# Performance work log

Hardware: AMD Instinct MI355X
Metric: run time of the kernel (lower is better)

## Reference

```python
import jax, jax.numpy as jnp
import numpy as np

D_X, D_K, D_V = 1024, 128, 128
B, N = 8, 2048


def setup_inputs() -> dict:
    key = jax.random.key(0)
    ks = jax.random.split(key, 7)
    s = lambda fan_in: 1.0 / np.sqrt(fan_in)
    return {
        "x": jax.random.normal(ks[0], (B, N, D_X), dtype=jnp.float32),
        "w_q": jax.random.uniform(ks[1], (D_K, D_X), jnp.float32, -s(D_X), s(D_X)),
        "b_q": jax.random.uniform(ks[2], (D_K,), jnp.float32, -s(D_X), s(D_X)),
        "w_k": jax.random.uniform(ks[3], (D_K, D_X), jnp.float32, -s(D_X), s(D_X)),
        "b_k": jax.random.uniform(ks[4], (D_K,), jnp.float32, -s(D_X), s(D_X)),
        "w_v": jax.random.uniform(ks[5], (D_V, D_X), jnp.float32, -s(D_X), s(D_X)),
        "b_v": jax.random.uniform(ks[6], (D_V,), jnp.float32, -s(D_X), s(D_X)),
    }


def reference(x, w_q, b_q, w_k, b_k, w_v, b_v):
    # Q is computed in the original module but unused; omit (no effect on output).
    K = jnp.einsum('bnx,kx->bnk', x, w_k) + b_k  # [B,N,d_k]
    V = jnp.einsum('bnx,vx->bnv', x, w_v) + b_v  # [B,N,d_v]
    # logits = K @ V^T / sqrt(d_k)  -> [B,N,N]  (note: K vs V, not Q vs K)
    scale = 1.0 / np.sqrt(D_K).astype(np.float32)
    logits = jnp.einsum('bnk,bmk->bnm', K, V) * scale
    attn = jax.nn.softmax(logits, axis=-1)
    return jnp.einsum('bnm,bmv->bnv', attn, V)
```

## Files before the change

### kernel.cpp

```cpp
#include <hip/hip_runtime.h>
#include <hip/hip_bf16.h>


typedef short s16x8 __attribute__((ext_vector_type(8)));
typedef float f32x4 __attribute__((ext_vector_type(4)));
typedef unsigned short u16;

#define AS1 __attribute__((address_space(1)))
#define AS3 __attribute__((address_space(3)))

__device__ __forceinline__ void gld_lds16(const void* g, void* l) {
  __builtin_amdgcn_global_load_lds((const AS1 unsigned int*)g, (AS3 unsigned int*)l, 16, 0, 0);
}

__device__ __forceinline__ float bf2f(u16 u) {
  unsigned int v = ((unsigned int)u) << 16;
  return __builtin_bit_cast(float, v);
}
__device__ __forceinline__ u16 f2bf(float f) {
  unsigned int u = __builtin_bit_cast(unsigned int, f);
  u += 0x7fffu + ((u >> 16) & 1u);
  return (u16)(u >> 16);
}
__device__ __forceinline__ unsigned pack_bf2(float a, float b) {
  unsigned ua = __builtin_bit_cast(unsigned, a) + 0x8000u;
  unsigned ub = __builtin_bit_cast(unsigned, b) + 0x8000u;
  return __builtin_amdgcn_perm(ub, ua, 0x07060302u);
}

__global__ __launch_bounds__(256, 4) void wconv_kernel(
    const float* __restrict__ wk, const float* __restrict__ wv,
    u16* __restrict__ wbf)
{
  const int e = (blockIdx.x * 256 + threadIdx.x) * 8;
  const float* src = (e < 131072) ? (wk + e) : (wv + (e - 131072));
  float4 a = *(const float4*)src;
  float4 b = *(const float4*)(src + 4);
  union { unsigned u[4]; s16x8 v; } pk;
  pk.u[0] = pack_bf2(a.x, a.y); pk.u[1] = pack_bf2(a.z, a.w);
  pk.u[2] = pack_bf2(b.x, b.y); pk.u[3] = pack_bf2(b.z, b.w);
  *(s16x8*)(wbf + e) = pk.v;
}

__global__ __launch_bounds__(512, 2) void kv_gemm_kernel(
    const float* __restrict__ x, const u16* __restrict__ wbf,
    const float* __restrict__ bk, const float* __restrict__ bv,
    u16* __restrict__ Kout, u16* __restrict__ Vout, u16* __restrict__ VTout)
{
  __shared__ u16 sA[2][8 * 512];
  __shared__ u16 sB[4][32 * 512];

  const int tid  = threadIdx.x;
  const int wave = tid >> 6;
  const int lane = tid & 63;
  const int l16  = lane & 15;
  const int lq   = lane >> 4;
  const int row0 = blockIdx.x * 64;
  const int wr   = wave >> 2;
  const int wc   = wave & 3;

  f32x4 acc[2][4];
  for (int i = 0; i < 2; ++i)
    for (int j = 0; j < 4; ++j) acc[i][j] = (f32x4){0.f, 0.f, 0.f, 0.f};

  const int kc = tid & 7, arow = tid >> 3;
  const float* aSrc = x + (size_t)(row0 + arow) * 1024 + kc * 8;
  const int aSlot = (((arow >> 4) * 2 + (kc >> 2)) * 512) + ((kc & 3) * 16 + (arow & 15)) * 8;

  const u16* bSrc[4];
  for (int i = 0; i < 4; ++i) {
    const int sl = wave + i * 8;
    bSrc[i] = wbf + (size_t)((sl >> 1) * 16 + l16) * 1024 + (sl & 1) * 32 + lq * 8;
  }

  for (int i = 0; i < 4; ++i)
    gld_lds16(bSrc[i], &sB[0][(wave + i * 8) * 512]);
  float4 p0a = *(const float4*)(aSrc);
  float4 p0b = *(const float4*)(aSrc + 4);
  for (int i = 0; i < 4; ++i)
    gld_lds16(bSrc[i] + 64, &sB[1][(wave + i * 8) * 512]);
  float4 p1a = *(const float4*)(aSrc + 64);
  float4 p1b = *(const float4*)(aSrc + 68);

#pragma unroll
  for (int s = 0; s < 16; ++s) {
    const int buf2 = s & 1, buf4 = s & 3;
    {
      union { unsigned u[4]; s16x8 v; } pk;
      pk.u[0] = pack_bf2(p0a.x, p0a.y); pk.u[1] = pack_bf2(p0a.z, p0a.w);
      pk.u[2] = pack_bf2(p0b.x, p0b.y); pk.u[3] = pack_bf2(p0b.z, p0b.w);
      *(s16x8*)(&sA[buf2][aSlot]) = pk.v;
    }
    asm volatile("s_waitcnt lgkmcnt(0)" ::: "memory");
    __builtin_amdgcn_s_barrier();
    if (s == 15) asm volatile("s_waitcnt vmcnt(0)" ::: "memory");
    else         asm volatile("s_waitcnt vmcnt(6)" ::: "memory");
    __builtin_amdgcn_sched_barrier(0);

    if (s + 2 < 16) {
      for (int i = 0; i < 4; ++i)
        gld_lds16(bSrc[i] + (s + 2) * 64, &sB[(s + 2) & 3][(wave + i * 8) * 512]);
    }
    p0a = p1a; p0b = p1b;
    if (s + 2 < 16) {
      p1a = *(const float4*)(aSrc + (s + 2) * 64);
      p1b = *(const float4*)(aSrc + (s + 2) * 64 + 4);
    }

    s16x8 af[2][2], bfr[4][2];
    for (int rb = 0; rb < 2; ++rb)
      for (int ks = 0; ks < 2; ++ks)
        af[rb][ks] = *(const s16x8*)(&sA[buf2][(((wr * 2 + rb) * 2 + ks) * 64 + lane) * 8]);
    for (int cb = 0; cb < 4; ++cb)
      for (int ks = 0; ks < 2; ++ks)
        bfr[cb][ks] = *(const s16x8*)(&sB[buf4][(((wc * 4 + cb) * 2 + ks) * 64 + lane) * 8]);
    for (int rb = 0; rb < 2; ++rb)
      for (int cb = 0; cb < 4; ++cb)
        for (int ks = 0; ks < 2; ++ks)
          acc[rb][cb] = __builtin_amdgcn_mfma_f32_16x16x32_bf16(af[rb][ks], bfr[cb][ks], acc[rb][cb], 0, 0, 0);
  }

  const int  colBase = wc * 64;
  const bool isV = (wc >= 2);
  const float vscale = isV ? 1.0f : 0.08838834764831845f;
  u16* outN = isV ? Vout : Kout;
  float fbias[4];
  for (int cb = 0; cb < 4; ++cb) {
    const int col = colBase + cb * 16 + l16;
    fbias[cb] = isV ? bv[col - 128] : bk[col];
  }
  for (int rb = 0; rb < 2; ++rb) {
    const int grow0 = row0 + wr * 32 + rb * 16 + lq * 4;
    for (int cb = 0; cb < 4; ++cb) {
      const int gcol = colBase + cb * 16 + l16;
      const int ocol = isV ? (gcol - 128) : gcol;
      union { u16 u[4]; unsigned long long ull; } pk;
      for (int r = 0; r < 4; ++r) {
        u16 h = f2bf((acc[rb][cb][r] + fbias[cb]) * vscale);
        outN[(size_t)(grow0 + r) * 128 + ocol] = h;
        pk.u[r] = h;
      }
      if (isV) {
        const int bidx = grow0 >> 11;
        const int n    = grow0 & 2047;
        *(unsigned long long*)(VTout + (size_t)bidx * 128 * 2048 + (size_t)ocol * 2048 + n) = pk.ull;
      }
    }
  }
}

__global__ __launch_bounds__(256, 2) void flash_kernel(
    const u16* __restrict__ Kmat, const u16* __restrict__ Vmat,
    const u16* __restrict__ VT, float* __restrict__ out,
    float* __restrict__ Opart, float* __restrict__ lbuf)
{
  __shared__ u16 sV[2][16 * 512];
  __shared__ u16 sVT[2][16 * 512];

  const int tid  = threadIdx.x;
  const int wave = tid >> 6;
  const int lane = tid & 63;
  const int l16  = lane & 15;
  const int lq   = lane >> 4;
  const int b    = blockIdx.y;
  const int q0   = blockIdx.x * 64;
  const int z    = blockIdx.z;
  const int ntiles = (2048 / gridDim.z) / 64;
  const int mstart = z * (2048 / gridDim.z);

  const int bq   = lq & 1;
  const bool ahi = (lq & 2) != 0;
  const int src0 = l16 + (2 * bq + 0) * 16;
  const int src1 = l16 + (2 * bq + 1) * 16;

  s16x8 kf[4];
  {
    const u16* Kb = Kmat + ((size_t)b * 2048 + q0 + wave * 16 + l16) * 128 + lq * 8;
    for (int ks = 0; ks < 4; ++ks) kf[ks] = *(const s16x8*)(Kb + ks * 32);
  }

  const u16* vSrc[4];  const u16* vtSrc[4];
  {
    const u16* Vb  = Vmat + (size_t)b * 2048 * 128;
    const u16* VTb = VT   + (size_t)b * 128 * 2048;
    for (int i = 0; i < 4; ++i) {
      const int sl = wave + i * 4;
      vSrc[i]  = Vb  + (size_t)((sl >> 2) * 16 + l16) * 128 + (sl & 3) * 32 + lq * 8;
      vtSrc[i] = VTb + (size_t)((sl >> 1) * 16 + l16) * 2048 + (sl & 1) * 32 + lq * 8;
    }
  }

  f32x4 oacc[8];
  for (int v = 0; v < 8; ++v) oacc[v] = (f32x4){0.f, 0.f, 0.f, 0.f};
  float lrow = 0.f;

  for (int i = 0; i < 4; ++i) {
    gld_lds16(vSrc[i] + (size_t)mstart * 128, &sV[0][(wave + i * 4) * 512]);
    gld_lds16(vtSrc[i] + mstart,              &sVT[0][(wave + i * 4) * 512]);
  }

  for (int mt = 0; mt < ntiles; ++mt) {
    const int buf = mt & 1;
    asm volatile("s_barrier" ::: "memory");
    if (mt + 1 < ntiles) {
      const int m1 = mstart + (mt + 1) * 64;
      for (int i = 0; i < 4; ++i) {
        gld_lds16(vSrc[i] + (size_t)m1 * 128, &sV[buf ^ 1][(wave + i * 4) * 512]);
        gld_lds16(vtSrc[i] + m1,              &sVT[buf ^ 1][(wave + i * 4) * 512]);
      }
      asm volatile("s_waitcnt vmcnt(8)" ::: "memory");
    } else {
      asm volatile("s_waitcnt vmcnt(0)" ::: "memory");
    }
    __builtin_amdgcn_sched_barrier(0);

    f32x4 sacc[4];
    for (int t = 0; t < 4; ++t) sacc[t] = (f32x4){0.f, 0.f, 0.f, 0.f};
    for (int ks = 0; ks < 4; ++ks)
      for (int t = 0; t < 4; ++t)
        sacc[t] = __builtin_amdgcn_mfma_f32_16x16x32_bf16(
            *(const s16x8*)(&sV[buf][(t * 4 + ks) * 512 + lane * 8]), kf[ks], sacc[t], 0, 0, 0);

    unsigned D[4][2];
    float rs = 0.f;
    for (int t = 0; t < 4; ++t)
      for (int p = 0; p < 2; ++p) {
        float e0 = __expf(sacc[t][2 * p]);
        float e1 = __expf(sacc[t][2 * p + 1]);
        unsigned d = pack_bf2(e0, e1);
        D[t][p] = d;
        rs += bf2f((u16)(d & 0xffffu)) + bf2f((u16)(d >> 16));
      }
    lrow += rs;

    s16x8 pa[2];
    for (int ksm = 0; ksm < 2; ++ksm) {
      union { unsigned u[4]; s16x8 v; } fr;
      {
        unsigned lo = __shfl((int)D[2 * ksm][0], src0);
        unsigned hi = __shfl((int)D[2 * ksm + 1][0], src0);
        fr.u[0] = ahi ? hi : lo;
      }
      {
        unsigned lo = __shfl((int)D[2 * ksm][1], src0);
        unsigned hi = __shfl((int)D[2 * ksm + 1][1], src0);
        fr.u[1] = ahi ? hi : lo;
      }
      {
        unsigned lo = __shfl((int)D[2 * ksm][0], src1);
        unsigned hi = __shfl((int)D[2 * ksm + 1][0], src1);
        fr.u[2] = ahi ? hi : lo;
      }
      {
        unsigned lo = __shfl((int)D[2 * ksm][1], src1);
        unsigned hi = __shfl((int)D[2 * ksm + 1][1], src1);
        fr.u[3] = ahi ? hi : lo;
      }
      pa[ksm] = fr.v;
    }

    for (int ksm = 0; ksm < 2; ++ksm)
      for (int v = 0; v < 8; ++v)
        oacc[v] = __builtin_amdgcn_mfma_f32_16x16x32_bf16(
            pa[ksm], *(const s16x8*)(&sVT[buf][(v * 2 + ksm) * 512 + lane * 8]), oacc[v], 0, 0, 0);
  }

  lrow += __shfl_xor(lrow, 16);
  lrow += __shfl_xor(lrow, 32);

  const size_t rowg = (size_t)b * 2048 + q0 + wave * 16;
  if (gridDim.z == 1) {
    for (int r = 0; r < 4; ++r) {
      const float inv = 1.f / __shfl(lrow, lq * 4 + r);
      for (int v = 0; v < 8; ++v)
        out[(rowg + lq * 4 + r) * 128 + v * 16 + l16] = oacc[v][r] * inv;
    }
  } else {
    float* Op = Opart + (size_t)z * 2097152;
    float* lp = lbuf + (size_t)z * 32768;
    for (int r = 0; r < 4; ++r)
      for (int v = 0; v < 8; ++v)
        Op[(rowg + lq * 4 + r) * 128 + v * 16 + l16] = oacc[v][r];
    if (lq == 0)
      lp[rowg + l16] = lrow;
  }
}

__global__ __launch_bounds__(256, 4) void combine_kernel(
    const float* __restrict__ Opart, const float* __restrict__ lbuf,
    float* __restrict__ out)
{
  const int idx = blockIdx.x * 256 + threadIdx.x;
  const int row = idx >> 5;
  const float4 o0 = ((const float4*)Opart)[idx];
  const float4 o1 = ((const float4*)(Opart + 2097152))[idx];
  const float inv = 1.f / (lbuf[row] + lbuf[32768 + row]);
  float4 o;
  o.x = (o0.x + o1.x) * inv;
  o.y = (o0.y + o1.y) * inv;
  o.z = (o0.z + o1.z) * inv;
  o.w = (o0.w + o1.w) * inv;
  ((float4*)out)[idx] = o;
}

extern "C" void kernel_launch(void* const* d_in, const int* in_sizes, int n_in,
                              void* d_out, int out_size, void* d_ws, size_t ws_size,
                              hipStream_t stream) {
  const float* x  = (const float*)d_in[0];
  const float* wk = (const float*)d_in[3];
  const float* bk = (const float*)d_in[4];
  const float* wv = (const float*)d_in[5];
  const float* bv = (const float*)d_in[6];

  u16* ws   = (u16*)d_ws;
  u16* wbf  = ws;
  u16* Kmat = ws + 262144;
  u16* Vmat = Kmat + (size_t)16384 * 128;
  u16* VTm  = Vmat + (size_t)16384 * 128;
  float* Opart = (float*)(VTm + (size_t)16384 * 128);
  float* lbuf  = Opart + 2 * 2097152;
  const bool split = ws_size >= (size_t)30200000;

  wconv_kernel<<<128, 256, 0, stream>>>(wk, wv, wbf);
  kv_gemm_kernel<<<256, 512, 0, stream>>>(x, wbf, bk, bv, Kmat, Vmat, VTm);
  if (split) {
    flash_kernel<<<dim3(32, 8, 2), 256, 0, stream>>>(Kmat, Vmat, VTm,
                                                     (float*)d_out, Opart, lbuf);
    combine_kernel<<<2048, 256, 0, stream>>>(Opart, lbuf, (float*)d_out);
  } else {
    flash_kernel<<<dim3(32, 8, 1), 256, 0, stream>>>(Kmat, Vmat, VTm,
                                                     (float*)d_out, Opart, lbuf);
  }
}
```

Measured before the change: 164.5 us.

## Load x operand directly into MFMA registers, bypassing shared-memory staging

The A operand (x rows) is now loaded by each wave straight from global memory in the MFMA fragment layout, converted to bf16 in registers, and fed to MFMA without going through the sA shared buffer. This removes the LDS write and read of A, the lgkmcnt wait and one sync role of the barrier. In exchange, each of the four column-waves sharing a row group redundantly loads the same x data (4x more global/L2 traffic for A), register pressure rises with the double-buffered float4 arrays, and the vmcnt counts were retuned.

```diff
diff --git a/kernel.cpp b/kernel.cpp
--- a/kernel.cpp
+++ b/kernel.cpp
@@ -47,7 +47,6 @@
     const float* __restrict__ bk, const float* __restrict__ bv,
     u16* __restrict__ Kout, u16* __restrict__ Vout, u16* __restrict__ VTout)
 {
-  __shared__ u16 sA[2][8 * 512];
   __shared__ u16 sB[4][32 * 512];
 
   const int tid  = threadIdx.x;
@@ -63,57 +62,67 @@
   for (int i = 0; i < 2; ++i)
     for (int j = 0; j < 4; ++j) acc[i][j] = (f32x4){0.f, 0.f, 0.f, 0.f};
 
-  const int kc = tid & 7, arow = tid >> 3;
-  const float* aSrc = x + (size_t)(row0 + arow) * 1024 + kc * 8;
-  const int aSlot = (((arow >> 4) * 2 + (kc >> 2)) * 512) + ((kc & 3) * 16 + (arow & 15)) * 8;
-
   const u16* bSrc[4];
   for (int i = 0; i < 4; ++i) {
     const int sl = wave + i * 8;
     bSrc[i] = wbf + (size_t)((sl >> 1) * 16 + l16) * 1024 + (sl & 1) * 32 + lq * 8;
   }
 
+  const float* aBase = x + (size_t)(row0 + wr * 32 + l16) * 1024 + lq * 8;
+
+  float4 aregs[2][4][2];
   for (int i = 0; i < 4; ++i)
     gld_lds16(bSrc[i], &sB[0][(wave + i * 8) * 512]);
-  float4 p0a = *(const float4*)(aSrc);
-  float4 p0b = *(const float4*)(aSrc + 4);
+  for (int rb = 0; rb < 2; ++rb)
+    for (int ks = 0; ks < 2; ++ks) {
+      const float* p = aBase + rb * 16384 + ks * 32;
+      aregs[0][rb * 2 + ks][0] = *(const float4*)(p);
+      aregs[0][rb * 2 + ks][1] = *(const float4*)(p + 4);
+    }
   for (int i = 0; i < 4; ++i)
     gld_lds16(bSrc[i] + 64, &sB[1][(wave + i * 8) * 512]);
-  float4 p1a = *(const float4*)(aSrc + 64);
-  float4 p1b = *(const float4*)(aSrc + 68);
+  for (int rb = 0; rb < 2; ++rb)
+    for (int ks = 0; ks < 2; ++ks) {
+      const float* p = aBase + rb * 16384 + 64 + ks * 32;
+      aregs[1][rb * 2 + ks][0] = *(const float4*)(p);
+      aregs[1][rb * 2 + ks][1] = *(const float4*)(p + 4);
+    }
 
 #pragma unroll
   for (int s = 0; s < 16; ++s) {
-    const int buf2 = s & 1, buf4 = s & 3;
-    {
-      union { unsigned u[4]; s16x8 v; } pk;
-      pk.u[0] = pack_bf2(p0a.x, p0a.y); pk.u[1] = pack_bf2(p0a.z, p0a.w);
-      pk.u[2] = pack_bf2(p0b.x, p0b.y); pk.u[3] = pack_bf2(p0b.z, p0b.w);
-      *(s16x8*)(&sA[buf2][aSlot]) = pk.v;
-    }
-    asm volatile("s_waitcnt lgkmcnt(0)" ::: "memory");
+    const int buf = s & 3;
+    const int gen = s & 1;
     __builtin_amdgcn_s_barrier();
-    if (s == 15) asm volatile("s_waitcnt vmcnt(0)" ::: "memory");
-    else         asm volatile("s_waitcnt vmcnt(6)" ::: "memory");
-    __builtin_amdgcn_sched_barrier(0);
-
-    if (s + 2 < 16) {
+    if (s + 2 < 16)
       for (int i = 0; i < 4; ++i)
         gld_lds16(bSrc[i] + (s + 2) * 64, &sB[(s + 2) & 3][(wave + i * 8) * 512]);
-    }
-    p0a = p1a; p0b = p1b;
-    if (s + 2 < 16) {
-      p1a = *(const float4*)(aSrc + (s + 2) * 64);
-      p1b = *(const float4*)(aSrc + (s + 2) * 64 + 4);
-    }
-
-    s16x8 af[2][2], bfr[4][2];
+    if (s <= 13)      asm volatile("s_waitcnt vmcnt(16)" ::: "memory");
+    else if (s == 14) asm volatile("s_waitcnt vmcnt(12)" ::: "memory");
+    else              asm volatile("s_waitcnt vmcnt(0)" ::: "memory");
+    __builtin_amdgcn_sched_barrier(0);
+
+    s16x8 af[2][2];
     for (int rb = 0; rb < 2; ++rb)
-      for (int ks = 0; ks < 2; ++ks)
-        af[rb][ks] = *(const s16x8*)(&sA[buf2][(((wr * 2 + rb) * 2 + ks) * 64 + lane) * 8]);
+      for (int ks = 0; ks < 2; ++ks) {
+        union { unsigned u[4]; s16x8 v; } pk;
+        const float4 lo = aregs[gen][rb * 2 + ks][0];
+        const float4 hi = aregs[gen][rb * 2 + ks][1];
+        pk.u[0] = pack_bf2(lo.x, lo.y); pk.u[1] = pack_bf2(lo.z, lo.w);
+        pk.u[2] = pack_bf2(hi.x, hi.y); pk.u[3] = pack_bf2(hi.z, hi.w);
+        af[rb][ks] = pk.v;
+      }
+    if (s + 2 < 16)
+      for (int rb = 0; rb < 2; ++rb)
+        for (int ks = 0; ks < 2; ++ks) {
+          const float* p = aBase + rb * 16384 + (s + 2) * 64 + ks * 32;
+          aregs[gen][rb * 2 + ks][0] = *(const float4*)(p);
+          aregs[gen][rb * 2 + ks][1] = *(const float4*)(p + 4);
+        }
+
+    s16x8 bfr[4][2];
     for (int cb = 0; cb < 4; ++cb)
       for (int ks = 0; ks < 2; ++ks)
-        bfr[cb][ks] = *(const s16x8*)(&sB[buf4][(((wc * 4 + cb) * 2 + ks) * 64 + lane) * 8]);
+        bfr[cb][ks] = *(const s16x8*)(&sB[buf][(((wc * 4 + cb) * 2 + ks) * 64 + lane) * 8]);
     for (int rb = 0; rb < 2; ++rb)
       for (int cb = 0; cb < 4; ++cb)
         for (int ks = 0; ks < 2; ++ks)
```

Measured after the change: 183.6 us. +11.6%, slower.
